# Optimization experiments

Hardware: AMD Instinct MI355X
Metric: run time of the kernel (lower is better)

## Reference

```python
import jax, jax.numpy as jnp
import numpy as np

B, N_E, E_DIM = 131072, 1024, 64
BETA = 0.25


def setup_inputs() -> dict:
    key = jax.random.key(0)
    kz, kw = jax.random.split(key)
    z = jax.random.normal(kz, (B, E_DIM), dtype=jnp.float32)
    # nn.Embedding init: uniform(-1/n_e, 1/n_e)
    emb_w = jax.random.uniform(kw, (N_E, E_DIM), dtype=jnp.float32,
                               minval=-1.0 / N_E, maxval=1.0 / N_E)
    return {"z": z, "emb_w": emb_w}


def reference(z, emb_w):
    beta = jnp.float32(BETA)
    # pairwise squared distances: [B, n_e]
    d = (jnp.sum(z * z, axis=1, keepdims=True)
         + jnp.sum(emb_w * emb_w, axis=1)
         - 2.0 * jnp.einsum('bd,nd->bn', z, emb_w))
    idx = jnp.argmin(d, axis=1)                      # [B]
    z_q = jnp.take(emb_w, idx, axis=0)               # [B, e_dim]
    # legacy=False branch
    loss = (beta * jnp.mean((jax.lax.stop_gradient(z_q) - z) ** 2)
            + jnp.mean((z_q - jax.lax.stop_gradient(z)) ** 2))
    # straight-through estimator
    z_q_st = z + jax.lax.stop_gradient(z_q - z)
    # torch.var is unbiased (ddof=1)
    v = jnp.var(idx.astype(jnp.float32), ddof=1)
    return (z_q_st, loss, idx, v)
```

## Files before the change

kernel.cpp:

```cpp
#include <hip/hip_runtime.h>
#include <stdint.h>


typedef __attribute__((ext_vector_type(8))) __bf16 bf16x8;
typedef __attribute__((ext_vector_type(4))) float f32x4;

#define NBLK 2048
#define NTHR 256
#define OUT_LOSS 8388608
#define OUT_IDX  8388609
#define OUT_VAR  8519681

#define WS_LOSS 0
#define WS_S1   8192
#define WS_S2   16384
#define WS_EFRAG 24576
#define WS_EE   (24576 + 131072)

__global__ void vq_prep(const float* __restrict__ emb, char* __restrict__ ws) {
  bf16x8* efrag = (bf16x8*)(ws + WS_EFRAG);
  float* eeoff = (float*)(ws + WS_EE);
  const int t = blockIdx.x;
  const int l = threadIdx.x;
  const int n = t * 16 + (l & 15);
  const int kb0 = (l >> 4) * 8;
  const float* er = emb + n * 64;
  for (int j = 0; j < 2; ++j) {
    const int kb = j * 32 + kb0;
    bf16x8 h;
#pragma unroll
    for (int i = 0; i < 8; ++i) h[i] = (__bf16)(-2.0f * er[kb + i]);
    efrag[(t * 2 + j) * 64 + l] = h;
  }
  if (l < 16) {
    const float* e2 = emb + (t * 16 + l) * 64;
    float s = 0.f;
#pragma unroll
    for (int d = 0; d < 64; ++d) s += e2[d] * e2[d];
    eeoff[t * 16 + l] = s + 0.5f;
  }
}

__global__ void __launch_bounds__(NTHR, 4) vq_main(
    const float* __restrict__ z, const float* __restrict__ emb,
    float* __restrict__ out, char* __restrict__ ws) {
  const int tid = threadIdx.x;
  const int wave = tid >> 6, lane = tid & 63;
  const int lr = lane & 15, ksl = lane >> 4;
  const int k0 = ksl * 8;
  const int row_base = blockIdx.x * 64;

  bf16x8 zf[4][2];
  float zz[4];
#pragma unroll
  for (int r = 0; r < 4; ++r) {
    const float* zr = z + (size_t)(row_base + r * 16 + lr) * 64;
    float s = 0.f;
#pragma unroll
    for (int j = 0; j < 2; ++j) {
      f32x4 v0 = *(const f32x4*)(zr + j * 32 + k0);
      f32x4 v1 = *(const f32x4*)(zr + j * 32 + k0 + 4);
      bf16x8 h;
#pragma unroll
      for (int i = 0; i < 4; ++i) {
        h[i] = (__bf16)v0[i]; h[4 + i] = (__bf16)v1[i];
        s += v0[i] * v0[i] + v1[i] * v1[i];
      }
      zf[r][j] = h;
    }
    zz[r] = s;
  }

  unsigned mkey[4];
#pragma unroll
  for (int r = 0; r < 4; ++r) mkey[r] = 0xFFFFFFFFu;

  const bf16x8* efrag = (const bf16x8*)(ws + WS_EFRAG);
  const f32x4* eeoff = (const f32x4*)(ws + WS_EE);
#pragma unroll 2
  for (int tt = 0; tt < 16; ++tt) {
    const int t = wave * 16 + tt;
    bf16x8 e0 = efrag[(t * 2 + 0) * 64 + lane];
    bf16x8 e1 = efrag[(t * 2 + 1) * 64 + lane];
    f32x4 ee = eeoff[t * 4 + ksl];
    const unsigned nb = (unsigned)(t * 16 + ksl * 4);
#pragma unroll
    for (int r = 0; r < 4; ++r) {
      f32x4 acc = __builtin_amdgcn_mfma_f32_16x16x32_bf16(e0, zf[r][0], ee, 0, 0, 0);
      acc = __builtin_amdgcn_mfma_f32_16x16x32_bf16(e1, zf[r][1], acc, 0, 0, 0);
#pragma unroll
      for (int j = 0; j < 4; ++j) {
        unsigned key = (__float_as_uint(acc[j]) & 0xFFFFFC00u) | (nb + j);
        mkey[r] = min(mkey[r], key);
      }
    }
  }

#pragma unroll
  for (int r = 0; r < 4; ++r) {
    mkey[r] = min(mkey[r], (unsigned)__shfl_xor((int)mkey[r], 16, 64));
    mkey[r] = min(mkey[r], (unsigned)__shfl_xor((int)mkey[r], 32, 64));
    zz[r] += __shfl_xor(zz[r], 16, 64);
    zz[r] += __shfl_xor(zz[r], 32, 64);
  }

  __shared__ unsigned skey[4][64];
  __shared__ float szz[64];
  __shared__ float sL[4];
  __shared__ int sA[4], sB[4];
  if (ksl == 0) {
#pragma unroll
    for (int r = 0; r < 4; ++r) {
      skey[wave][r * 16 + lr] = mkey[r];
      if (wave == 0) szz[r * 16 + lr] = zz[r];
    }
  }
  __syncthreads();

  const int row = tid >> 2, seg = tid & 3;
  const unsigned k = min(min(skey[0][row], skey[1][row]),
                         min(skey[2][row], skey[3][row]));
  const unsigned idx = k & 1023u;
  const size_t rowg = (size_t)row_base + row;
  const f32x4* ep = (const f32x4*)(emb + (size_t)idx * 64 + seg * 16);
  f32x4* op = (f32x4*)(out + rowg * 64 + seg * 16);
#pragma unroll
  for (int c = 0; c < 4; ++c) op[c] = ep[c];

  float ls = 0.f; int s1 = 0, s2 = 0;
  if (seg == 0) {
    ls = szz[row] + __uint_as_float(k & 0xFFFFFC00u) - 0.5f;
    s1 = (int)idx;
    s2 = (int)(idx * idx);
    out[OUT_IDX + rowg] = (float)idx;
  }
#pragma unroll
  for (int off = 1; off < 64; off <<= 1) {
    ls += __shfl_xor(ls, off, 64);
    s1 += __shfl_xor(s1, off, 64);
    s2 += __shfl_xor(s2, off, 64);
  }
  if (lane == 0) { sL[wave] = ls; sA[wave] = s1; sB[wave] = s2; }
  __syncthreads();
  if (tid == 0) {
    float L = 0; int a = 0, b = 0;
#pragma unroll
    for (int w = 0; w < 4; ++w) { L += sL[w]; a += sA[w]; b += sB[w]; }
    ((float*)(ws + WS_LOSS))[blockIdx.x] = L;
    ((int*)(ws + WS_S1))[blockIdx.x] = a;
    ((int*)(ws + WS_S2))[blockIdx.x] = b;
  }
}

__global__ void vq_final(float* __restrict__ out, const char* __restrict__ ws) {
  const int t = threadIdx.x;
  const float* lp = (const float*)(ws + WS_LOSS);
  const int* p1 = (const int*)(ws + WS_S1);
  const int* p2 = (const int*)(ws + WS_S2);
  double L = 0; long long a = 0, b = 0;
#pragma unroll
  for (int kk = 0; kk < 8; ++kk) {
    const int i = t + 256 * kk;
    L += (double)lp[i];
    a += (long long)p1[i];
    b += (long long)p2[i];
  }
#pragma unroll
  for (int off = 1; off < 64; off <<= 1) {
    L += __shfl_xor(L, off, 64);
    a += __shfl_xor(a, off, 64);
    b += __shfl_xor(b, off, 64);
  }
  __shared__ double sL[4];
  __shared__ long long sA[4], sB[4];
  const int wave = t >> 6, lane = t & 63;
  if (lane == 0) { sL[wave] = L; sA[wave] = a; sB[wave] = b; }
  __syncthreads();
  if (t == 0) {
    double Lt = 0; long long at = 0, bt = 0;
#pragma unroll
    for (int w = 0; w < 4; ++w) { Lt += sL[w]; at += sA[w]; bt += sB[w]; }
    out[OUT_LOSS] = (float)(1.25 * Lt / 8388608.0);
    long long num = bt * 131072LL - at * at;
    out[OUT_VAR] = (float)((double)num / (131072.0 * 131071.0));
  }
}

extern "C" void kernel_launch(void* const* d_in, const int* in_sizes, int n_in,
                              void* d_out, int out_size, void* d_ws, size_t ws_size,
                              hipStream_t stream) {
  (void)in_sizes; (void)n_in; (void)out_size; (void)ws_size;
  const float* z = (const float*)d_in[0];
  const float* emb = (const float*)d_in[1];
  float* out = (float*)d_out;
  char* ws = (char*)d_ws;
  vq_prep<<<64, 64, 0, stream>>>(emb, ws);
  vq_main<<<NBLK, NTHR, 0, stream>>>(z, emb, out, ws);
  vq_final<<<1, 256, 0, stream>>>(out, ws);
}
```

Before: 55.45 us.

## Stage codebook in LDS and switch to 32x32x16 MFMA with bias-row trick

The main kernel now uses 256 blocks of 512 threads. Each block copies the whole bf16 codebook fragment set (128 KB) plus the norm fragments into LDS with global_load_lds, instead of having each wave read its slice from global memory. Each wave covers 64 rows against all 1024 codes using 32x32x16 MFMAs, and an extra MFMA adds ||e||^2 through a ones column. The argmin is done within the lane, and each lane then writes a full output row. This cuts global codebook traffic and reduction shuffles, but occupancy drops to one large-LDS block per CU, and the wave count and instruction mix change substantially.

```diff
diff --git a/kernel.cpp b/kernel.cpp
--- a/kernel.cpp
+++ b/kernel.cpp
@@ -4,136 +4,166 @@
 
 typedef __attribute__((ext_vector_type(8))) __bf16 bf16x8;
 typedef __attribute__((ext_vector_type(4))) float f32x4;
-
-#define NBLK 2048
-#define NTHR 256
+typedef __attribute__((ext_vector_type(16))) float f32x16;
+
 #define OUT_LOSS 8388608
 #define OUT_IDX  8388609
 #define OUT_VAR  8519681
 
-#define WS_LOSS 0
-#define WS_S1   8192
-#define WS_S2   16384
-#define WS_EFRAG 24576
-#define WS_EE   (24576 + 131072)
+#define WS_LOSS  0
+#define WS_S1    4096
+#define WS_S2    8192
+#define WS_EFRAG 12288
+#define WS_A4    143360
+
+__device__ __forceinline__ void gld_lds16(const void* g, void* l) {
+  __builtin_amdgcn_global_load_lds(
+      (const __attribute__((address_space(1))) unsigned*)g,
+      (__attribute__((address_space(3))) unsigned*)l, 16, 0, 0);
+}
 
 __global__ void vq_prep(const float* __restrict__ emb, char* __restrict__ ws) {
   bf16x8* efrag = (bf16x8*)(ws + WS_EFRAG);
-  float* eeoff = (float*)(ws + WS_EE);
+  bf16x8* a4 = (bf16x8*)(ws + WS_A4);
   const int t = blockIdx.x;
   const int l = threadIdx.x;
-  const int n = t * 16 + (l & 15);
-  const int kb0 = (l >> 4) * 8;
+  const int n = t * 32 + (l & 31);
+  const int kb = (l >> 5) * 8;
   const float* er = emb + n * 64;
-  for (int j = 0; j < 2; ++j) {
-    const int kb = j * 32 + kb0;
+#pragma unroll
+  for (int ks = 0; ks < 4; ++ks) {
     bf16x8 h;
 #pragma unroll
-    for (int i = 0; i < 8; ++i) h[i] = (__bf16)(-2.0f * er[kb + i]);
-    efrag[(t * 2 + j) * 64 + l] = h;
-  }
-  if (l < 16) {
-    const float* e2 = emb + (t * 16 + l) * 64;
+    for (int i = 0; i < 8; ++i) h[i] = (__bf16)(-2.0f * er[ks * 16 + kb + i]);
+    efrag[(t * 4 + ks) * 64 + l] = h;
+  }
+  if (l < 32) {
     float s = 0.f;
 #pragma unroll
-    for (int d = 0; d < 64; ++d) s += e2[d] * e2[d];
-    eeoff[t * 16 + l] = s + 0.5f;
-  }
-}
-
-__global__ void __launch_bounds__(NTHR, 4) vq_main(
+    for (int d = 0; d < 64; ++d) s += er[d] * er[d];
+    bf16x8 h;
+#pragma unroll
+    for (int i = 0; i < 8; ++i) h[i] = (__bf16)0.f;
+    h[0] = (__bf16)s;
+    a4[t * 32 + l] = h;
+  }
+}
+
+__global__ void __launch_bounds__(512) vq_main(
     const float* __restrict__ z, const float* __restrict__ emb,
     float* __restrict__ out, char* __restrict__ ws) {
+  __shared__ char sfrag[131072];
+  __shared__ char sa4[16384];
+  __shared__ float sL[8];
+  __shared__ int sA[8], sB[8];
+
   const int tid = threadIdx.x;
   const int wave = tid >> 6, lane = tid & 63;
-  const int lr = lane & 15, ksl = lane >> 4;
-  const int k0 = ksl * 8;
-  const int row_base = blockIdx.x * 64;
-
-  bf16x8 zf[4][2];
-  float zz[4];
-#pragma unroll
-  for (int r = 0; r < 4; ++r) {
-    const float* zr = z + (size_t)(row_base + r * 16 + lr) * 64;
+  const int l31 = lane & 31, lh = lane >> 5;
+  const int rb = blockIdx.x * 512 + wave * 64;
+
+#pragma unroll
+  for (int i = 0; i < 16; ++i)
+    gld_lds16(ws + WS_EFRAG + i * 8192 + wave * 1024 + lane * 16,
+              sfrag + i * 8192 + wave * 1024);
+#pragma unroll
+  for (int i = 0; i < 2; ++i)
+    gld_lds16(ws + WS_A4 + i * 8192 + wave * 1024 + lane * 16,
+              sa4 + i * 8192 + wave * 1024);
+
+  bf16x8 zb[2][4];
+  float zzp[2];
+#pragma unroll
+  for (int rg = 0; rg < 2; ++rg) {
+    const float* zp = z + (size_t)(rb + rg * 32 + l31) * 64 + lh * 8;
     float s = 0.f;
 #pragma unroll
-    for (int j = 0; j < 2; ++j) {
-      f32x4 v0 = *(const f32x4*)(zr + j * 32 + k0);
-      f32x4 v1 = *(const f32x4*)(zr + j * 32 + k0 + 4);
+    for (int ks = 0; ks < 4; ++ks) {
+      f32x4 v0 = *(const f32x4*)(zp + ks * 16);
+      f32x4 v1 = *(const f32x4*)(zp + ks * 16 + 4);
       bf16x8 h;
 #pragma unroll
       for (int i = 0; i < 4; ++i) {
         h[i] = (__bf16)v0[i]; h[4 + i] = (__bf16)v1[i];
         s += v0[i] * v0[i] + v1[i] * v1[i];
       }
-      zf[r][j] = h;
+      zb[rg][ks] = h;
     }
-    zz[r] = s;
-  }
-
-  unsigned mkey[4];
-#pragma unroll
-  for (int r = 0; r < 4; ++r) mkey[r] = 0xFFFFFFFFu;
-
-  const bf16x8* efrag = (const bf16x8*)(ws + WS_EFRAG);
-  const f32x4* eeoff = (const f32x4*)(ws + WS_EE);
-#pragma unroll 2
-  for (int tt = 0; tt < 16; ++tt) {
-    const int t = wave * 16 + tt;
-    bf16x8 e0 = efrag[(t * 2 + 0) * 64 + lane];
-    bf16x8 e1 = efrag[(t * 2 + 1) * 64 + lane];
-    f32x4 ee = eeoff[t * 4 + ksl];
-    const unsigned nb = (unsigned)(t * 16 + ksl * 4);
-#pragma unroll
-    for (int r = 0; r < 4; ++r) {
-      f32x4 acc = __builtin_amdgcn_mfma_f32_16x16x32_bf16(e0, zf[r][0], ee, 0, 0, 0);
-      acc = __builtin_amdgcn_mfma_f32_16x16x32_bf16(e1, zf[r][1], acc, 0, 0, 0);
-#pragma unroll
-      for (int j = 0; j < 4; ++j) {
-        unsigned key = (__float_as_uint(acc[j]) & 0xFFFFFC00u) | (nb + j);
-        mkey[r] = min(mkey[r], key);
-      }
-    }
-  }
-
-#pragma unroll
-  for (int r = 0; r < 4; ++r) {
-    mkey[r] = min(mkey[r], (unsigned)__shfl_xor((int)mkey[r], 16, 64));
-    mkey[r] = min(mkey[r], (unsigned)__shfl_xor((int)mkey[r], 32, 64));
-    zz[r] += __shfl_xor(zz[r], 16, 64);
-    zz[r] += __shfl_xor(zz[r], 32, 64);
-  }
-
-  __shared__ unsigned skey[4][64];
-  __shared__ float szz[64];
-  __shared__ float sL[4];
-  __shared__ int sA[4], sB[4];
-  if (ksl == 0) {
-#pragma unroll
-    for (int r = 0; r < 4; ++r) {
-      skey[wave][r * 16 + lr] = mkey[r];
-      if (wave == 0) szz[r * 16 + lr] = zz[r];
-    }
-  }
+    zzp[rg] = s;
+  }
+  bf16x8 zb4;
+#pragma unroll
+  for (int i = 0; i < 8; ++i) zb4[i] = (__bf16)0.f;
+  if (lh == 0) zb4[0] = (__bf16)1.0f;
+
+  f32x16 half16;
+#pragma unroll
+  for (int i = 0; i < 16; ++i) half16[i] = 0.5f;
+
+  asm volatile("s_waitcnt vmcnt(0)" ::: "memory");
   __syncthreads();
 
-  const int row = tid >> 2, seg = tid & 3;
-  const unsigned k = min(min(skey[0][row], skey[1][row]),
-                         min(skey[2][row], skey[3][row]));
-  const unsigned idx = k & 1023u;
-  const size_t rowg = (size_t)row_base + row;
-  const f32x4* ep = (const f32x4*)(emb + (size_t)idx * 64 + seg * 16);
-  f32x4* op = (f32x4*)(out + rowg * 64 + seg * 16);
-#pragma unroll
-  for (int c = 0; c < 4; ++c) op[c] = ep[c];
-
-  float ls = 0.f; int s1 = 0, s2 = 0;
-  if (seg == 0) {
-    ls = szz[row] + __uint_as_float(k & 0xFFFFFC00u) - 0.5f;
-    s1 = (int)idx;
-    s2 = (int)(idx * idx);
-    out[OUT_IDX + rowg] = (float)idx;
-  }
+  const bf16x8* fr = (const bf16x8*)sfrag;
+  const bf16x8* a4 = (const bf16x8*)sa4;
+  unsigned rk0 = 0xFFFFFFFFu, rk1 = 0xFFFFFFFFu;
+  const unsigned vbase = 4u * (unsigned)lh;
+
+#pragma unroll
+  for (int t = 0; t < 32; ++t) {
+    const bf16x8 A0 = fr[(t * 4 + 0) * 64 + lane];
+    const bf16x8 A1 = fr[(t * 4 + 1) * 64 + lane];
+    const bf16x8 A2 = fr[(t * 4 + 2) * 64 + lane];
+    const bf16x8 A3 = fr[(t * 4 + 3) * 64 + lane];
+    const bf16x8 A4v = a4[t * 32 + l31];
+    __builtin_amdgcn_s_setprio(1);
+    f32x16 c0 = __builtin_amdgcn_mfma_f32_32x32x16_bf16(A0, zb[0][0], half16, 0, 0, 0);
+    c0 = __builtin_amdgcn_mfma_f32_32x32x16_bf16(A1, zb[0][1], c0, 0, 0, 0);
+    c0 = __builtin_amdgcn_mfma_f32_32x32x16_bf16(A2, zb[0][2], c0, 0, 0, 0);
+    c0 = __builtin_amdgcn_mfma_f32_32x32x16_bf16(A3, zb[0][3], c0, 0, 0, 0);
+    c0 = __builtin_amdgcn_mfma_f32_32x32x16_bf16(A4v, zb4, c0, 0, 0, 0);
+    f32x16 c1 = __builtin_amdgcn_mfma_f32_32x32x16_bf16(A0, zb[1][0], half16, 0, 0, 0);
+    c1 = __builtin_amdgcn_mfma_f32_32x32x16_bf16(A1, zb[1][1], c1, 0, 0, 0);
+    c1 = __builtin_amdgcn_mfma_f32_32x32x16_bf16(A2, zb[1][2], c1, 0, 0, 0);
+    c1 = __builtin_amdgcn_mfma_f32_32x32x16_bf16(A3, zb[1][3], c1, 0, 0, 0);
+    c1 = __builtin_amdgcn_mfma_f32_32x32x16_bf16(A4v, zb4, c1, 0, 0, 0);
+    __builtin_amdgcn_s_setprio(0);
+    unsigned q[16];
+#pragma unroll
+    for (int r = 0; r < 16; ++r)
+      q[r] = (__float_as_uint(c0[r]) & 0xFFFFFC00u) | (unsigned)((r & 3) + 8 * (r >> 2));
+#pragma unroll
+    for (int s = 8; s > 0; s >>= 1)
+#pragma unroll
+      for (int i = 0; i < 8; ++i) if (i < s) q[i] = min(q[i], q[i + s]);
+    rk0 = min(rk0, q[0] + vbase + (unsigned)(t * 32));
+#pragma unroll
+    for (int r = 0; r < 16; ++r)
+      q[r] = (__float_as_uint(c1[r]) & 0xFFFFFC00u) | (unsigned)((r & 3) + 8 * (r >> 2));
+#pragma unroll
+    for (int s = 8; s > 0; s >>= 1)
+#pragma unroll
+      for (int i = 0; i < 8; ++i) if (i < s) q[i] = min(q[i], q[i + s]);
+    rk1 = min(rk1, q[0] + vbase + (unsigned)(t * 32));
+  }
+
+  rk0 = min(rk0, (unsigned)__shfl_xor((int)rk0, 32, 64));
+  rk1 = min(rk1, (unsigned)__shfl_xor((int)rk1, 32, 64));
+  float zz0 = zzp[0] + __shfl_xor(zzp[0], 32, 64);
+  float zz1 = zzp[1] + __shfl_xor(zzp[1], 32, 64);
+
+  const unsigned key = (lane < 32) ? rk0 : rk1;
+  const float zzv = (lane < 32) ? zz0 : zz1;
+  const unsigned idx = key & 1023u;
+  const size_t rowg = (size_t)rb + lane;
+  const f32x4* ep = (const f32x4*)(emb + (size_t)idx * 64);
+  f32x4* op = (f32x4*)(out + rowg * 64);
+#pragma unroll
+  for (int c = 0; c < 16; ++c) op[c] = ep[c];
+  out[OUT_IDX + rowg] = (float)idx;
+
+  float ls = zzv + __uint_as_float(key & 0xFFFFFC00u) - 0.5f;
+  int s1 = (int)idx;
+  int s2 = (int)(idx * idx);
 #pragma unroll
   for (int off = 1; off < 64; off <<= 1) {
     ls += __shfl_xor(ls, off, 64);
@@ -145,7 +175,7 @@
   if (tid == 0) {
     float L = 0; int a = 0, b = 0;
 #pragma unroll
-    for (int w = 0; w < 4; ++w) { L += sL[w]; a += sA[w]; b += sB[w]; }
+    for (int w = 0; w < 8; ++w) { L += sL[w]; a += sA[w]; b += sB[w]; }
     ((float*)(ws + WS_LOSS))[blockIdx.x] = L;
     ((int*)(ws + WS_S1))[blockIdx.x] = a;
     ((int*)(ws + WS_S2))[blockIdx.x] = b;
@@ -157,29 +187,24 @@
   const float* lp = (const float*)(ws + WS_LOSS);
   const int* p1 = (const int*)(ws + WS_S1);
   const int* p2 = (const int*)(ws + WS_S2);
-  double L = 0; long long a = 0, b = 0;
-#pragma unroll
-  for (int kk = 0; kk < 8; ++kk) {
-    const int i = t + 256 * kk;
-    L += (double)lp[i];
-    a += (long long)p1[i];
-    b += (long long)p2[i];
-  }
+  double L = (double)lp[t];
+  long long a = (long long)p1[t];
+  long long b = (long long)p2[t];
 #pragma unroll
   for (int off = 1; off < 64; off <<= 1) {
     L += __shfl_xor(L, off, 64);
     a += __shfl_xor(a, off, 64);
     b += __shfl_xor(b, off, 64);
   }
-  __shared__ double sL[4];
-  __shared__ long long sA[4], sB[4];
+  __shared__ double sLf[4];
+  __shared__ long long sAf[4], sBf[4];
   const int wave = t >> 6, lane = t & 63;
-  if (lane == 0) { sL[wave] = L; sA[wave] = a; sB[wave] = b; }
+  if (lane == 0) { sLf[wave] = L; sAf[wave] = a; sBf[wave] = b; }
   __syncthreads();
   if (t == 0) {
     double Lt = 0; long long at = 0, bt = 0;
 #pragma unroll
-    for (int w = 0; w < 4; ++w) { Lt += sL[w]; at += sA[w]; bt += sB[w]; }
+    for (int w = 0; w < 4; ++w) { Lt += sLf[w]; at += sAf[w]; bt += sBf[w]; }
     out[OUT_LOSS] = (float)(1.25 * Lt / 8388608.0);
     long long num = bt * 131072LL - at * at;
     out[OUT_VAR] = (float)((double)num / (131072.0 * 131071.0));
@@ -194,7 +219,7 @@
   const float* emb = (const float*)d_in[1];
   float* out = (float*)d_out;
   char* ws = (char*)d_ws;
-  vq_prep<<<64, 64, 0, stream>>>(emb, ws);
-  vq_main<<<NBLK, NTHR, 0, stream>>>(z, emb, out, ws);
+  vq_prep<<<32, 64, 0, stream>>>(emb, ws);
+  vq_main<<<256, 512, 0, stream>>>(z, emb, out, ws);
   vq_final<<<1, 256, 0, stream>>>(out, ws);
 }
```

After: 45.07 us. -18.7%, faster.
